# Optimization experiments

Hardware: AMD Instinct MI355X
Metric: run time of the kernel (lower is better)

Reference implementation:

```python
import jax, jax.numpy as jnp
import numpy as np

B, S, E = 4, 2048, 512
H, D = 8, 64
MIN_W, MAX_W = 256, 1024
EPS = 1e-6


def setup_inputs() -> dict:
    key = jax.random.key(0)
    ks = jax.random.split(key, 9)
    w = lambda k, shp: jax.random.normal(k, shp, dtype=jnp.float32) * 0.02
    return {
        "x": jax.random.normal(ks[0], (B, S, E), dtype=jnp.float32),
        "rms1_w": jnp.ones((E,), jnp.float32),
        "rms2_w": jnp.ones((E,), jnp.float32),
        "qkv_w": w(ks[1], (3 * E, E)),
        "out_w": w(ks[2], (E, E)),
        "cs_w1": w(ks[3], (E // 4, E)),
        "cs_w2": w(ks[4], (1, E // 4)),
        "gate_w": w(ks[5], (2304, E)),
        "up_w": w(ks[6], (2304, E)),
        "down_w": w(ks[7], (E, 2304)),
    }


def _rmsnorm(x, w):
    rms = jax.lax.rsqrt(jnp.mean(x * x, axis=-1, keepdims=True) + EPS)
    return x * rms * w


def _rotate_half(x):
    x1 = x[..., ::2]
    x2 = x[..., 1::2]
    return jnp.stack((-x2, x1), axis=-1).reshape(x.shape)


def reference(x, rms1_w, rms2_w, qkv_w, out_w, cs_w1, cs_w2, gate_w, up_w, down_w):
    # --- pre-norm ---
    h = _rmsnorm(x, rms1_w)                                  # [B,S,E]
    # --- qkv ---
    qkv = h @ qkv_w.T                                        # [B,S,3E]
    qkv = qkv.reshape(B, S, 3, H, D).transpose(2, 0, 3, 1, 4)
    q, k, v = qkv[0], qkv[1], qkv[2]                         # [B,H,S,D]
    # --- RoPE (cat-freqs cos/sin + interleaved rotate_half, as in source) ---
    inv_freq = 1.0 / (10000.0 ** (jnp.arange(0, D, 2, dtype=jnp.float32) / D))
    pos = jnp.arange(S, dtype=jnp.float32)
    freqs = jnp.outer(pos, inv_freq)                         # [S,D/2]
    emb = jnp.concatenate([freqs, freqs], axis=-1)           # [S,D]
    cos = jnp.cos(emb)[None, None]
    sin = jnp.sin(emb)[None, None]
    q = q * cos + _rotate_half(q) * sin
    k = k * cos + _rotate_half(k) * sin
    # --- attention scores ---
    scale = D ** -0.5
    scores = jnp.einsum("bhqd,bhkd->bhqk", q, k) * scale     # [B,H,S,S]
    # --- complexity -> dynamic window size ---
    n = S * E
    mu = jnp.mean(h, axis=(1, 2), keepdims=True)
    var = jnp.sum((h - mu) ** 2, axis=(1, 2)) / (n - 1)      # unbiased, per batch
    var_norm = jax.nn.sigmoid(var * 10.0 - 5.0)
    xm = jnp.mean(h, axis=1)                                 # [B,E]
    learned = jax.nn.sigmoid((jax.nn.silu(xm @ cs_w1.T)) @ cs_w2.T)[:, 0]
    complexity = (var_norm + learned) / 2.0                  # [B]
    ws_f = MIN_W + jnp.mean(complexity) * (MAX_W - MIN_W)
    ws = ws_f.astype(jnp.int32)                              # trunc, like .int()
    ws = jnp.maximum(jnp.minimum(ws, S), MIN_W)
    # --- causal + sliding-window mask ---
    p = jnp.arange(S)
    rel = p[:, None] - p[None, :]                            # [S,S]
    allowed = (rel >= 0) & (rel < ws)
    scores = jnp.where(allowed[None, None], scores, -jnp.inf)
    attn = jax.nn.softmax(scores, axis=-1)
    out = jnp.einsum("bhqk,bhkd->bhqd", attn, v)             # [B,H,S,D]
    out = out.transpose(0, 2, 1, 3).reshape(B, S, E)
    out = out @ out_w.T
    x = x + out
    # --- SwiGLU FFN ---
    h2 = _rmsnorm(x, rms2_w)
    ffn = (jax.nn.silu(h2 @ gate_w.T) * (h2 @ up_w.T)) @ down_w.T
    return x + ffn
```

## Files before the change

### kernel.cpp

```cpp
#include <hip/hip_runtime.h>

typedef unsigned short u16;
typedef unsigned int   u32;
typedef __attribute__((ext_vector_type(4))) float  f32x4;
typedef __attribute__((ext_vector_type(8))) __bf16 bf16x8;
typedef __attribute__((ext_vector_type(4))) u32    u32x4;
typedef __attribute__((ext_vector_type(2))) u32    u32x2;

#define B_ 4
#define S_ 2048
#define E_ 512
#define H_ 8
#define D_ 64

__device__ __forceinline__ u16 f2bf(float f) {
  union { float f; u32 u; } a; a.f = f;
  u32 r = a.u + 0x7FFFu + ((a.u >> 16) & 1u);
  return (u16)(r >> 16);
}
__device__ __forceinline__ float bf2f(u16 u) {
  union { u32 u; float f; } a; a.u = (u32)u << 16;
  return a.f;
}
__device__ __forceinline__ u32 pkbf(float lo, float hi) {
  u32 r;
  asm("v_cvt_pk_bf16_f32 %0, %1, %2" : "=v"(r) : "v"(lo), "v"(hi));
  return r;
}

#define GLOAD16(gp, lp) __builtin_amdgcn_global_load_lds( \
    (const __attribute__((address_space(1))) void*)(gp),  \
    (__attribute__((address_space(3))) void*)(lp), 16, 0, 0)

#define BARRIER() asm volatile("s_barrier" ::: "memory")

__global__ __launch_bounds__(256) void cvt_k(const float* __restrict__ s,
                                             u16* __restrict__ d, int n) {
  int i = (blockIdx.x * 256 + threadIdx.x) * 4;
  if (i >= n) return;
  f32x4 v = *(const f32x4*)(s + i);
  u32x2 o;
  o.x = pkbf(v[0], v[1]);
  o.y = pkbf(v[2], v[3]);
  *(u32x2*)(d + i) = o;
}

__global__ __launch_bounds__(256) void ropetab_k(float* __restrict__ ct,
                                                 float* __restrict__ st) {
  int idx = blockIdx.x * 256 + threadIdx.x;
  int s = idx >> 6, j = idx & 63;
  float f = powf(10000.f, -(float)(j & 31) * (1.f / 32.f));
  float ang = (float)s * f;
  ct[idx] = cosf(ang);
  st[idx] = sinf(ang);
}

__global__ __launch_bounds__(256) void rmsnorm_k(const float* __restrict__ x,
                                                 const float* __restrict__ wv,
                                                 u16* __restrict__ o) {
  const int row = blockIdx.x;
  const int t = threadIdx.x;
  const float* xr = x + (size_t)row * E_;
  float v0 = xr[t], v1 = xr[t + 256];
  float ss = v0 * v0 + v1 * v1;
#pragma unroll
  for (int m = 1; m < 64; m <<= 1) ss += __shfl_xor(ss, m, 64);
  __shared__ float red[4];
  if ((t & 63) == 0) red[t >> 6] = ss;
  __syncthreads();
  float tot = red[0] + red[1] + red[2] + red[3];
  float rms = 1.f / sqrtf(tot * (1.f / (float)E_) + 1e-6f);
  o[(size_t)row * E_ + t]       = f2bf(v0 * rms * wv[t]);
  o[(size_t)row * E_ + t + 256] = f2bf(v1 * rms * wv[t + 256]);
}

__global__ __launch_bounds__(256) void colsum_k(const u16* __restrict__ h,
                                                float* __restrict__ st) {
  const int b = blockIdx.x >> 3, ck = blockIdx.x & 7;
  const u16* hb = h + ((size_t)b * S_ + ck * 256) * E_;
  const int t = threadIdx.x;
  float a0 = 0, a1 = 0, s = 0, sq = 0;
  for (int r = 0; r < 256; ++r) {
    float v0 = bf2f(hb[(size_t)r * E_ + t]);
    float v1 = bf2f(hb[(size_t)r * E_ + t + 256]);
    a0 += v0; a1 += v1;
    s += v0 + v1; sq += v0 * v0 + v1 * v1;
  }
  atomicAdd(&st[8 + b * E_ + t], a0);
  atomicAdd(&st[8 + b * E_ + t + 256], a1);
#pragma unroll
  for (int m = 1; m < 64; m <<= 1) { s += __shfl_xor(s, m, 64); sq += __shfl_xor(sq, m, 64); }
  if ((t & 63) == 0) { atomicAdd(&st[b], s); atomicAdd(&st[4 + b], sq); }
}

__global__ __launch_bounds__(128) void wscalc_k(float* __restrict__ st,
                                                const float* __restrict__ w1,
                                                const float* __restrict__ w2) {
  const int j = threadIdx.x;
  __shared__ float comp[4];
  __shared__ float tw[2];
  float dot[4] = {0.f, 0.f, 0.f, 0.f};
  const float* w1r = w1 + (size_t)j * E_;
  for (int e = 0; e < E_; ++e) {
    float wv = w1r[e];
    dot[0] += st[8 + 0 * E_ + e] * wv;
    dot[1] += st[8 + 1 * E_ + e] * wv;
    dot[2] += st[8 + 2 * E_ + e] * wv;
    dot[3] += st[8 + 3 * E_ + e] * wv;
  }
  for (int b = 0; b < 4; ++b) {
    float d = dot[b] * (1.f / (float)S_);
    float si = d / (1.f + __expf(-d));
    float term = si * w2[j];
#pragma unroll
    for (int m = 1; m < 64; m <<= 1) term += __shfl_xor(term, m, 64);
    __syncthreads();
    if ((j & 63) == 0) tw[j >> 6] = term;
    __syncthreads();
    if (j == 0) {
      float pre = tw[0] + tw[1];
      float learned = 1.f / (1.f + __expf(-pre));
      const float n = (float)S_ * (float)E_;
      float sum = st[b], ssq = st[4 + b];
      float var = (ssq - sum * sum / n) / (n - 1.f);
      float vn = 1.f / (1.f + __expf(-(var * 10.f - 5.f)));
      comp[b] = 0.5f * (vn + learned);
    }
    __syncthreads();
  }
  if (j == 0) {
    float mean = 0.25f * (comp[0] + comp[1] + comp[2] + comp[3]);
    float wsf = 256.f + mean * 768.f;
    int v = (int)wsf;
    v = v < 256 ? 256 : (v > S_ ? S_ : v);
    ((int*)st)[2056] = v;
  }
}

struct EpiArgs {
  u16* q; u16* k; u16* vt;
  const float* cosT; const float* sinT;
  const float* resid; float* outf;
};

template <int N, int K, int EPI, int WAVES>
__global__ __launch_bounds__(WAVES * 64) void gemm_k(const u16* __restrict__ A,
                                                     const u16* __restrict__ W,
                                                     EpiArgs ea) {
  constexpr int NBN = N / 128;
  __shared__ u16 sA[2][128 * 32];
  __shared__ u16 sB[2][128 * 32];
  const int tid = threadIdx.x;
  const int nwg = (int)gridDim.x;
  const int bid = (int)blockIdx.x;
  const int logical = (bid & 7) * (nwg >> 3) + (bid >> 3);
  const int bm = logical / NBN, bn = logical % NBN;
  const int lane = tid & 63, w = tid >> 6;
  const int g = lane >> 4, c = lane & 15;
  constexpr int MI = (WAVES == 4) ? 4 : 2;
  const int wrow = (w >> 1) * ((WAVES == 4) ? 64 : 32);
  const int wcol = (w & 1) * 64;

  const int sr0 = w * 16 + (lane >> 2);
  const int ch0 = (lane & 3) ^ ((sr0 >> 1) & 3);
  const u16* gA = A + (size_t)(bm * 128 + sr0) * K + ch0 * 8;
  const u16* gB = W + (size_t)(bn * 128 + sr0) * K + ch0 * 8;
  const int lofs = w * 1024;

  f32x4 acc[MI][4];
  f32x4 zz = {0.f, 0.f, 0.f, 0.f};
#pragma unroll
  for (int i = 0; i < MI; ++i)
#pragma unroll
    for (int j = 0; j < 4; ++j) acc[i][j] = zz;

  auto stage = [&](int buf, int ko) {
    GLOAD16(gA + ko, (char*)sA[buf] + lofs);
    GLOAD16(gB + ko, (char*)sB[buf] + lofs);
    if constexpr (WAVES == 4) {
      GLOAD16(gA + (size_t)64 * K + ko, (char*)sA[buf] + lofs + 4096);
      GLOAD16(gB + (size_t)64 * K + ko, (char*)sB[buf] + lofs + 4096);
    }
  };

  constexpr int NIT = K / 32;
  stage(0, 0);
  int cur = 0;
  for (int it = 0; it < NIT; ++it) {
    if (it + 1 < NIT) {
      stage(cur ^ 1, (it + 1) * 32);
      if constexpr (WAVES == 4) asm volatile("s_waitcnt vmcnt(4)" ::: "memory");
      else                      asm volatile("s_waitcnt vmcnt(2)" ::: "memory");
    } else {
      asm volatile("s_waitcnt vmcnt(0)" ::: "memory");
    }
    BARRIER();
    const u16* bufA = sA[cur];
    const u16* bufB = sB[cur];
    bf16x8 af[MI], bfr[4];
#pragma unroll
    for (int mi = 0; mi < MI; ++mi) {
      int ar = wrow + mi * 16 + c;
      af[mi] = *(const bf16x8*)&bufA[ar * 32 + ((g ^ ((ar >> 1) & 3)) * 8)];
    }
#pragma unroll
    for (int nj = 0; nj < 4; ++nj) {
      int br = wcol + nj * 16 + c;
      bfr[nj] = *(const bf16x8*)&bufB[br * 32 + ((g ^ ((br >> 1) & 3)) * 8)];
    }
#pragma unroll
    for (int mi = 0; mi < MI; ++mi)
#pragma unroll
      for (int nj = 0; nj < 4; ++nj)
        acc[mi][nj] = __builtin_amdgcn_mfma_f32_16x16x32_bf16(af[mi], bfr[nj], acc[mi][nj], 0, 0, 0);
    BARRIER();
    cur ^= 1;
  }

#pragma unroll
  for (int mi = 0; mi < MI; ++mi) {
#pragma unroll
    for (int nj = 0; nj < 4; ++nj) {
      const int rowb = bm * 128 + wrow + mi * 16 + 4 * g;
      const int cc = bn * 128 + wcol + nj * 16 + c;
      if constexpr (EPI == 0) {
        const int which = cc >> 9;
        const int hh = (cc >> 6) & 7;
        const int d = cc & 63;
        const int bi = rowb >> 11;
        const int s = rowb & (S_ - 1);
        if (which == 2) {
          u32x2 pk;
          pk.x = pkbf(acc[mi][nj][0], acc[mi][nj][1]);
          pk.y = pkbf(acc[mi][nj][2], acc[mi][nj][3]);
          *(u32x2*)(ea.vt + (((size_t)(bi * H_ + hh) * D_ + d) * S_ + s)) = pk;
        } else {
          u16* dst = (which == 0 ? ea.q : ea.k) + (((size_t)(bi * H_ + hh) * S_ + s) * D_ + d);
#pragma unroll
          for (int r = 0; r < 4; ++r) {
            float v = acc[mi][nj][r];
            float pv = __shfl_xor(v, 1, 64);
            int si = s + r;
            float cs = ea.cosT[si * 64 + d];
            float sn = ea.sinT[si * 64 + d];
            float o = v * cs + ((d & 1) ? pv : -pv) * sn;
            dst[(size_t)r * D_] = f2bf(o);
          }
        }
      } else {
#pragma unroll
        for (int r = 0; r < 4; ++r) {
          size_t idx = (size_t)(rowb + r) * N + cc;
          ea.outf[idx] = acc[mi][nj][r] + ea.resid[idx];
        }
      }
    }
  }
}

__global__ __launch_bounds__(512) void gemmgu_k(const u16* __restrict__ A,
                                                const u16* __restrict__ Wg,
                                                const u16* __restrict__ Wu,
                                                u16* __restrict__ outb) {
  __shared__ u16 sA[2][128 * 32];
  __shared__ u16 sG[2][128 * 32];
  __shared__ u16 sU[2][128 * 32];
  const int tid = threadIdx.x;
  const int nwg = (int)gridDim.x;
  const int bid = (int)blockIdx.x;
  const int logical = (bid & 7) * (nwg >> 3) + (bid >> 3);
  const int bm = logical / 18, bn = logical % 18;
  const int lane = tid & 63, w = tid >> 6;
  const int g = lane >> 4, c = lane & 15;
  const int wrow = (w >> 1) * 32;
  const int wcol = (w & 1) * 64;

  const int sr0 = w * 16 + (lane >> 2);
  const int ch0 = (lane & 3) ^ ((sr0 >> 1) & 3);
  const u16* gA = A + (size_t)(bm * 128 + sr0) * 512 + ch0 * 8;
  const u16* gG = Wg + (size_t)(bn * 128 + sr0) * 512 + ch0 * 8;
  const u16* gU = Wu + (size_t)(bn * 128 + sr0) * 512 + ch0 * 8;
  const int lofs = w * 1024;

  f32x4 accg[2][4], accu[2][4];
  f32x4 zz = {0.f, 0.f, 0.f, 0.f};
#pragma unroll
  for (int i = 0; i < 2; ++i)
#pragma unroll
    for (int j = 0; j < 4; ++j) { accg[i][j] = zz; accu[i][j] = zz; }

  auto stage = [&](int buf, int ko) {
    GLOAD16(gA + ko, (char*)sA[buf] + lofs);
    GLOAD16(gG + ko, (char*)sG[buf] + lofs);
    GLOAD16(gU + ko, (char*)sU[buf] + lofs);
  };

  stage(0, 0);
  int cur = 0;
  for (int it = 0; it < 16; ++it) {
    if (it + 1 < 16) {
      stage(cur ^ 1, (it + 1) * 32);
      asm volatile("s_waitcnt vmcnt(3)" ::: "memory");
    } else {
      asm volatile("s_waitcnt vmcnt(0)" ::: "memory");
    }
    BARRIER();
    const u16* bufA = sA[cur];
    const u16* bufG = sG[cur];
    const u16* bufU = sU[cur];
    bf16x8 af[2], bg[4], bu[4];
#pragma unroll
    for (int mi = 0; mi < 2; ++mi) {
      int ar = wrow + mi * 16 + c;
      af[mi] = *(const bf16x8*)&bufA[ar * 32 + ((g ^ ((ar >> 1) & 3)) * 8)];
    }
#pragma unroll
    for (int nj = 0; nj < 4; ++nj) {
      int br = wcol + nj * 16 + c;
      int sw = (g ^ ((br >> 1) & 3)) * 8;
      bg[nj] = *(const bf16x8*)&bufG[br * 32 + sw];
      bu[nj] = *(const bf16x8*)&bufU[br * 32 + sw];
    }
#pragma unroll
    for (int mi = 0; mi < 2; ++mi)
#pragma unroll
      for (int nj = 0; nj < 4; ++nj) {
        accg[mi][nj] = __builtin_amdgcn_mfma_f32_16x16x32_bf16(af[mi], bg[nj], accg[mi][nj], 0, 0, 0);
        accu[mi][nj] = __builtin_amdgcn_mfma_f32_16x16x32_bf16(af[mi], bu[nj], accu[mi][nj], 0, 0, 0);
      }
    BARRIER();
    cur ^= 1;
  }

#pragma unroll
  for (int mi = 0; mi < 2; ++mi) {
#pragma unroll
    for (int nj = 0; nj < 4; ++nj) {
      const int rowb = bm * 128 + wrow + mi * 16 + 4 * g;
      const int cc = bn * 128 + wcol + nj * 16 + c;
#pragma unroll
      for (int r = 0; r < 4; ++r) {
        float gv = accg[mi][nj][r];
        float uv = accu[mi][nj][r];
        float sil = gv / (1.f + __expf(-gv));
        outb[(size_t)(rowb + r) * 2304 + cc] = f2bf(sil * uv);
      }
    }
  }
}

__global__ __launch_bounds__(128) void attn_k(const u16* __restrict__ Qb,
                                              const u16* __restrict__ Kb,
                                              const u16* __restrict__ Vt,
                                              u16* __restrict__ ao,
                                              const int* __restrict__ wsp) {
  const int bid = (int)blockIdx.x;
  const int qh = 63 - (bid >> 5);
  const int bh = bid & 31;
  const int b = bh >> 3, h = bh & 7;
  const int tid = threadIdx.x;
  const int w = tid >> 6, lane = tid & 63;
  const int g = lane >> 4, c = lane & 15;
  const int ws = *wsp;
  const int qw = qh * 32 + w * 16;
  const u16* Qh = Qb + (size_t)bh * S_ * D_;
  const u16* Kh = Kb + (size_t)bh * S_ * D_;
  const u16* Vh = Vt + (size_t)bh * D_ * S_;

  bf16x8 qf0 = *(const bf16x8*)(Qh + (qw + c) * D_ + g * 8);
  bf16x8 qf1 = *(const bf16x8*)(Qh + (qw + c) * D_ + 32 + g * 8);

  const float SCL = 0.125f * 1.44269504089f;
  float m2 = -3e38f, lsum = 0.f;
  f32x4 O[4];
  f32x4 zz = {0.f, 0.f, 0.f, 0.f};
#pragma unroll
  for (int i = 0; i < 4; ++i) O[i] = zz;

  int lo = qw - ws + 1;
  if (lo < 0) lo = 0;
  const int q = qw + c;
  for (int kb = lo & ~63; kb <= qw + 15; kb += 64) {
    bf16x8 kf[4][2];
#pragma unroll
    for (int t = 0; t < 4; ++t) {
      const u16* kp = Kh + (kb + 16 * t + c) * D_;
      kf[t][0] = *(const bf16x8*)(kp + g * 8);
      kf[t][1] = *(const bf16x8*)(kp + 32 + g * 8);
    }
    f32x4 st4[4];
    __builtin_amdgcn_s_setprio(1);
#pragma unroll
    for (int t = 0; t < 4; ++t) {
      f32x4 s = zz;
      s = __builtin_amdgcn_mfma_f32_16x16x32_bf16(kf[t][0], qf0, s, 0, 0, 0);
      s = __builtin_amdgcn_mfma_f32_16x16x32_bf16(kf[t][1], qf1, s, 0, 0, 0);
      st4[t] = s;
    }
    __builtin_amdgcn_s_setprio(0);
    bf16x8 vf[4][2];
#pragma unroll
    for (int dt = 0; dt < 4; ++dt) {
      const u16* vp = Vh + (size_t)(dt * 16 + c) * S_ + kb;
      vf[dt][0] = *(const bf16x8*)(vp + g * 8);
      vf[dt][1] = *(const bf16x8*)(vp + 32 + g * 8);
    }
    const bool interior = (kb + 63 <= qw) && (kb >= qw + 16 - ws);
    float p[4][4];
    float bm = -3e38f;
    if (interior) {
#pragma unroll
      for (int t = 0; t < 4; ++t)
#pragma unroll
        for (int r = 0; r < 4; ++r) {
          p[t][r] = st4[t][r] * SCL;
          bm = fmaxf(bm, p[t][r]);
        }
    } else {
#pragma unroll
      for (int t = 0; t < 4; ++t)
#pragma unroll
        for (int r = 0; r < 4; ++r) {
          int ki = kb + 16 * t + 4 * g + r;
          float v = st4[t][r] * SCL;
          bool ok = (q >= ki) && (q - ki) < ws;
          p[t][r] = ok ? v : -__builtin_inff();
          bm = fmaxf(bm, p[t][r]);
        }
    }
    bm = fmaxf(bm, __shfl_xor(bm, 16, 64));
    bm = fmaxf(bm, __shfl_xor(bm, 32, 64));
    if (!__all(bm - m2 <= 8.f)) {
      float mnew = fmaxf(m2, bm);
      float al = exp2f(m2 - mnew);
      lsum *= al;
#pragma unroll
      for (int i = 0; i < 4; ++i) O[i] *= al;
      m2 = mnew;
    }
    float psum = 0.f;
#pragma unroll
    for (int t = 0; t < 4; ++t)
#pragma unroll
      for (int r = 0; r < 4; ++r) {
        p[t][r] = exp2f(p[t][r] - m2);
        psum += p[t][r];
      }
    psum += __shfl_xor(psum, 16, 64);
    psum += __shfl_xor(psum, 32, 64);
    lsum += psum;

    u32 pp[4][2];
#pragma unroll
    for (int t = 0; t < 4; ++t) {
      pp[t][0] = pkbf(p[t][0], p[t][1]);
      pp[t][1] = pkbf(p[t][2], p[t][3]);
    }
    const int lA = (g & 1) * 32 + c;
    const int lB = lA + 16;
    const int hi = g >> 1;
    union { bf16x8 v; u32 u[4]; } pf0, pf1;
#pragma unroll
    for (int wi = 0; wi < 2; ++wi) {
      u32 a0 = (u32)__shfl((int)pp[0][wi], lA, 64);
      u32 a1 = (u32)__shfl((int)pp[1][wi], lA, 64);
      u32 a2 = (u32)__shfl((int)pp[2][wi], lA, 64);
      u32 a3 = (u32)__shfl((int)pp[3][wi], lA, 64);
      u32 b0 = (u32)__shfl((int)pp[0][wi], lB, 64);
      u32 b1 = (u32)__shfl((int)pp[1][wi], lB, 64);
      u32 b2 = (u32)__shfl((int)pp[2][wi], lB, 64);
      u32 b3 = (u32)__shfl((int)pp[3][wi], lB, 64);
      pf0.u[wi]     = hi ? a1 : a0;
      pf0.u[2 + wi] = hi ? b1 : b0;
      pf1.u[wi]     = hi ? a3 : a2;
      pf1.u[2 + wi] = hi ? b3 : b2;
    }
    __builtin_amdgcn_s_setprio(1);
#pragma unroll
    for (int dt = 0; dt < 4; ++dt) {
      O[dt] = __builtin_amdgcn_mfma_f32_16x16x32_bf16(vf[dt][0], pf0.v, O[dt], 0, 0, 0);
      O[dt] = __builtin_amdgcn_mfma_f32_16x16x32_bf16(vf[dt][1], pf1.v, O[dt], 0, 0, 0);
    }
    __builtin_amdgcn_s_setprio(0);
  }

  float inv = 1.f / lsum;
  __shared__ u16 ob[2][16][80];
#pragma unroll
  for (int dt = 0; dt < 4; ++dt)
#pragma unroll
    for (int r = 0; r < 4; ++r)
      ob[w][c][dt * 16 + 4 * g + r] = f2bf(O[dt][r] * inv);
  __syncthreads();
#pragma unroll
  for (int it = 0; it < 2; ++it) {
    int linear = tid + it * 128;
    int qrow = linear >> 3, ch = linear & 7;
    u32x4 v = *(const u32x4*)&ob[qrow >> 4][qrow & 15][ch * 8];
    *(u32x4*)(ao + ((size_t)(b * S_ + qh * 32 + qrow)) * E_ + h * D_ + ch * 8) = v;
  }
}

extern "C" void kernel_launch(void* const* d_in, const int* in_sizes, int n_in,
                              void* d_out, int out_size, void* d_ws, size_t ws_size,
                              hipStream_t stream) {
  const float* x      = (const float*)d_in[0];
  const float* rms1_w = (const float*)d_in[1];
  const float* rms2_w = (const float*)d_in[2];
  const float* qkv_w  = (const float*)d_in[3];
  const float* out_w  = (const float*)d_in[4];
  const float* cs_w1  = (const float*)d_in[5];
  const float* cs_w2  = (const float*)d_in[6];
  const float* gate_w = (const float*)d_in[7];
  const float* up_w   = (const float*)d_in[8];
  const float* down_w = (const float*)d_in[9];

  char* ws = (char*)d_ws;
  constexpr size_t o_wqkv = 0;
  constexpr size_t o_wout = 1572864;
  constexpr size_t o_wgate = 2097152;
  constexpr size_t o_wup = 4456448;
  constexpr size_t o_wdown = 6815744;
  constexpr size_t o_h = 9175040;
  constexpr size_t o_stats = 17563648;
  constexpr size_t o_cos = 17580032;
  constexpr size_t o_sin = 18104320;
  constexpr size_t o_Q = 18628608;
  constexpr size_t o_K = 27017216;
  constexpr size_t o_Vt = 35405824;
  constexpr size_t o_x2 = 43794432;
  constexpr size_t o_gate = 60571648;

  u16* wqkv = (u16*)(ws + o_wqkv);
  u16* wout = (u16*)(ws + o_wout);
  u16* wgate = (u16*)(ws + o_wgate);
  u16* wup = (u16*)(ws + o_wup);
  u16* wdown = (u16*)(ws + o_wdown);
  u16* h = (u16*)(ws + o_h);
  float* stats = (float*)(ws + o_stats);
  float* cosT = (float*)(ws + o_cos);
  float* sinT = (float*)(ws + o_sin);
  u16* Qb = (u16*)(ws + o_Q);
  u16* Kb = (u16*)(ws + o_K);
  u16* Vt = (u16*)(ws + o_Vt);
  float* x2 = (float*)(ws + o_x2);
  u16* gateb = (u16*)(ws + o_gate);
  u16* attno = h;
  u16* h2 = Qb;

  hipMemsetAsync(stats, 0, 16384, stream);
  cvt_k<<<768, 256, 0, stream>>>(qkv_w, wqkv, 1536 * 512);
  cvt_k<<<256, 256, 0, stream>>>(out_w, wout, 512 * 512);
  cvt_k<<<1152, 256, 0, stream>>>(gate_w, wgate, 2304 * 512);
  cvt_k<<<1152, 256, 0, stream>>>(up_w, wup, 2304 * 512);
  cvt_k<<<1152, 256, 0, stream>>>(down_w, wdown, 512 * 2304);
  ropetab_k<<<512, 256, 0, stream>>>(cosT, sinT);

  rmsnorm_k<<<8192, 256, 0, stream>>>(x, rms1_w, h);
  colsum_k<<<32, 256, 0, stream>>>(h, stats);
  wscalc_k<<<1, 128, 0, stream>>>(stats, cs_w1, cs_w2);

  EpiArgs ea{};
  ea.q = Qb; ea.k = Kb; ea.vt = Vt; ea.cosT = cosT; ea.sinT = sinT;
  gemm_k<1536, 512, 0, 4><<<768, 256, 0, stream>>>(h, wqkv, ea);

  attn_k<<<2048, 128, 0, stream>>>(Qb, Kb, Vt, attno, (const int*)(stats + 2056));

  EpiArgs e2{};
  e2.resid = x; e2.outf = x2;
  gemm_k<512, 512, 1, 8><<<256, 512, 0, stream>>>(attno, wout, e2);

  rmsnorm_k<<<8192, 256, 0, stream>>>(x2, rms2_w, h2);

  gemmgu_k<<<1152, 512, 0, stream>>>(h2, wgate, wup, gateb);

  EpiArgs e5{};
  e5.resid = x2; e5.outf = (float*)d_out;
  gemm_k<512, 2304, 1, 8><<<256, 512, 0, stream>>>(gateb, wdown, e5);

  (void)in_sizes; (void)n_in; (void)out_size; (void)ws_size;
}
```

Measured before the change: 397.0 us.

## Merge prep kernels, widen GEMM K-tile to 64, stage attention K/V in LDS

Merges the five weight-conversion launches and the RoPE table launch into one prep kernel. The GEMM now always runs 8 waves with a 64-wide K step, a double-buffered LDS tile and an XOR swizzle, which halves the number of barrier iterations. Attention moves to 64-query blocks of 4 waves that share K/V tiles staged through double-buffered LDS with async global-to-LDS loads, where before each wave read K/V straight from global memory. The trade-offs are more LDS per block, an extra barrier and full vmcnt wait per K block, and fewer attention blocks in the grid.

```diff
diff --git a/kernel.cpp b/kernel.cpp
--- a/kernel.cpp
+++ b/kernel.cpp
@@ -34,25 +34,37 @@
 
 #define BARRIER() asm volatile("s_barrier" ::: "memory")
 
-__global__ __launch_bounds__(256) void cvt_k(const float* __restrict__ s,
-                                             u16* __restrict__ d, int n) {
-  int i = (blockIdx.x * 256 + threadIdx.x) * 4;
-  if (i >= n) return;
+__global__ __launch_bounds__(256) void prep_k(const float* __restrict__ qkv_w,
+                                              const float* __restrict__ out_w,
+                                              const float* __restrict__ gate_w,
+                                              const float* __restrict__ up_w,
+                                              const float* __restrict__ down_w,
+                                              u16* __restrict__ wqkv, u16* __restrict__ wout,
+                                              u16* __restrict__ wgate, u16* __restrict__ wup,
+                                              u16* __restrict__ wdown,
+                                              float* __restrict__ ct, float* __restrict__ st) {
+  int bid = (int)blockIdx.x;
+  const float* s; u16* d; int base;
+  if (bid < 768)       { s = qkv_w;  d = wqkv;  base = bid; }
+  else if (bid < 1024) { s = out_w;  d = wout;  base = bid - 768; }
+  else if (bid < 2176) { s = gate_w; d = wgate; base = bid - 1024; }
+  else if (bid < 3328) { s = up_w;   d = wup;   base = bid - 2176; }
+  else if (bid < 4480) { s = down_w; d = wdown; base = bid - 3328; }
+  else {
+    int idx = (bid - 4480) * 256 + threadIdx.x;
+    int sp = idx >> 6, j = idx & 63;
+    float f = powf(10000.f, -(float)(j & 31) * (1.f / 32.f));
+    float ang = (float)sp * f;
+    ct[idx] = cosf(ang);
+    st[idx] = sinf(ang);
+    return;
+  }
+  int i = (base * 256 + threadIdx.x) * 4;
   f32x4 v = *(const f32x4*)(s + i);
   u32x2 o;
   o.x = pkbf(v[0], v[1]);
   o.y = pkbf(v[2], v[3]);
   *(u32x2*)(d + i) = o;
-}
-
-__global__ __launch_bounds__(256) void ropetab_k(float* __restrict__ ct,
-                                                 float* __restrict__ st) {
-  int idx = blockIdx.x * 256 + threadIdx.x;
-  int s = idx >> 6, j = idx & 63;
-  float f = powf(10000.f, -(float)(j & 31) * (1.f / 32.f));
-  float ang = (float)s * f;
-  ct[idx] = cosf(ang);
-  st[idx] = sinf(ang);
 }
 
 __global__ __launch_bounds__(256) void rmsnorm_k(const float* __restrict__ x,
@@ -143,13 +155,13 @@
   const float* resid; float* outf;
 };
 
-template <int N, int K, int EPI, int WAVES>
-__global__ __launch_bounds__(WAVES * 64) void gemm_k(const u16* __restrict__ A,
-                                                     const u16* __restrict__ W,
-                                                     EpiArgs ea) {
+template <int N, int K, int EPI>
+__global__ __launch_bounds__(512) void gemm_k(const u16* __restrict__ A,
+                                              const u16* __restrict__ W,
+                                              EpiArgs ea) {
   constexpr int NBN = N / 128;
-  __shared__ u16 sA[2][128 * 32];
-  __shared__ u16 sB[2][128 * 32];
+  __shared__ u16 sA[2][128 * 64];
+  __shared__ u16 sB[2][128 * 64];
   const int tid = threadIdx.x;
   const int nwg = (int)gridDim.x;
   const int bid = (int)blockIdx.x;
@@ -157,68 +169,69 @@
   const int bm = logical / NBN, bn = logical % NBN;
   const int lane = tid & 63, w = tid >> 6;
   const int g = lane >> 4, c = lane & 15;
-  constexpr int MI = (WAVES == 4) ? 4 : 2;
-  const int wrow = (w >> 1) * ((WAVES == 4) ? 64 : 32);
+  const int wrow = (w >> 1) * 32;
   const int wcol = (w & 1) * 64;
 
-  const int sr0 = w * 16 + (lane >> 2);
-  const int ch0 = (lane & 3) ^ ((sr0 >> 1) & 3);
-  const u16* gA = A + (size_t)(bm * 128 + sr0) * K + ch0 * 8;
-  const u16* gB = W + (size_t)(bn * 128 + sr0) * K + ch0 * 8;
-  const int lofs = w * 1024;
-
-  f32x4 acc[MI][4];
+  const int lr0 = lane >> 3;
+  const int scol = ((lane & 7) ^ lr0) * 8;
+  const u16* gA = A + (size_t)(bm * 128 + w * 16 + lr0) * K + scol;
+  const u16* gB = W + (size_t)(bn * 128 + w * 16 + lr0) * K + scol;
+
+  f32x4 acc[2][4];
   f32x4 zz = {0.f, 0.f, 0.f, 0.f};
 #pragma unroll
-  for (int i = 0; i < MI; ++i)
+  for (int i = 0; i < 2; ++i)
 #pragma unroll
     for (int j = 0; j < 4; ++j) acc[i][j] = zz;
 
   auto stage = [&](int buf, int ko) {
-    GLOAD16(gA + ko, (char*)sA[buf] + lofs);
-    GLOAD16(gB + ko, (char*)sB[buf] + lofs);
-    if constexpr (WAVES == 4) {
-      GLOAD16(gA + (size_t)64 * K + ko, (char*)sA[buf] + lofs + 4096);
-      GLOAD16(gB + (size_t)64 * K + ko, (char*)sB[buf] + lofs + 4096);
-    }
+    GLOAD16(gA + ko,                (char*)sA[buf] + (w * 16) * 128);
+    GLOAD16(gA + (size_t)8 * K + ko, (char*)sA[buf] + (w * 16 + 8) * 128);
+    GLOAD16(gB + ko,                (char*)sB[buf] + (w * 16) * 128);
+    GLOAD16(gB + (size_t)8 * K + ko, (char*)sB[buf] + (w * 16 + 8) * 128);
   };
 
-  constexpr int NIT = K / 32;
+  constexpr int NIT = K / 64;
   stage(0, 0);
   int cur = 0;
   for (int it = 0; it < NIT; ++it) {
     if (it + 1 < NIT) {
-      stage(cur ^ 1, (it + 1) * 32);
-      if constexpr (WAVES == 4) asm volatile("s_waitcnt vmcnt(4)" ::: "memory");
-      else                      asm volatile("s_waitcnt vmcnt(2)" ::: "memory");
+      stage(cur ^ 1, (it + 1) * 64);
+      asm volatile("s_waitcnt vmcnt(4)" ::: "memory");
     } else {
       asm volatile("s_waitcnt vmcnt(0)" ::: "memory");
     }
     BARRIER();
     const u16* bufA = sA[cur];
     const u16* bufB = sB[cur];
-    bf16x8 af[MI], bfr[4];
-#pragma unroll
-    for (int mi = 0; mi < MI; ++mi) {
+    bf16x8 af[2][2], bfr[4][2];
+#pragma unroll
+    for (int mi = 0; mi < 2; ++mi) {
       int ar = wrow + mi * 16 + c;
-      af[mi] = *(const bf16x8*)&bufA[ar * 32 + ((g ^ ((ar >> 1) & 3)) * 8)];
+#pragma unroll
+      for (int kk = 0; kk < 2; ++kk)
+        af[mi][kk] = *(const bf16x8*)&bufA[ar * 64 + (((kk * 4 + g) ^ (ar & 7)) * 8)];
     }
 #pragma unroll
     for (int nj = 0; nj < 4; ++nj) {
       int br = wcol + nj * 16 + c;
-      bfr[nj] = *(const bf16x8*)&bufB[br * 32 + ((g ^ ((br >> 1) & 3)) * 8)];
-    }
-#pragma unroll
-    for (int mi = 0; mi < MI; ++mi)
-#pragma unroll
-      for (int nj = 0; nj < 4; ++nj)
-        acc[mi][nj] = __builtin_amdgcn_mfma_f32_16x16x32_bf16(af[mi], bfr[nj], acc[mi][nj], 0, 0, 0);
+#pragma unroll
+      for (int kk = 0; kk < 2; ++kk)
+        bfr[nj][kk] = *(const bf16x8*)&bufB[br * 64 + (((kk * 4 + g) ^ (br & 7)) * 8)];
+    }
+#pragma unroll
+    for (int kk = 0; kk < 2; ++kk)
+#pragma unroll
+      for (int mi = 0; mi < 2; ++mi)
+#pragma unroll
+        for (int nj = 0; nj < 4; ++nj)
+          acc[mi][nj] = __builtin_amdgcn_mfma_f32_16x16x32_bf16(af[mi][kk], bfr[nj][kk], acc[mi][nj], 0, 0, 0);
     BARRIER();
     cur ^= 1;
   }
 
 #pragma unroll
-  for (int mi = 0; mi < MI; ++mi) {
+  for (int mi = 0; mi < 2; ++mi) {
 #pragma unroll
     for (int nj = 0; nj < 4; ++nj) {
       const int rowb = bm * 128 + wrow + mi * 16 + 4 * g;
@@ -349,26 +362,33 @@
   }
 }
 
-__global__ __launch_bounds__(128) void attn_k(const u16* __restrict__ Qb,
+__global__ __launch_bounds__(256) void attn_k(const u16* __restrict__ Qb,
                                               const u16* __restrict__ Kb,
                                               const u16* __restrict__ Vt,
                                               u16* __restrict__ ao,
                                               const int* __restrict__ wsp) {
+  __shared__ u16 sK[2][64 * 64];
+  __shared__ u16 sV[2][64 * 64];
   const int bid = (int)blockIdx.x;
-  const int qh = 63 - (bid >> 5);
+  const int qt = 31 - (bid >> 5);
   const int bh = bid & 31;
   const int b = bh >> 3, h = bh & 7;
   const int tid = threadIdx.x;
   const int w = tid >> 6, lane = tid & 63;
   const int g = lane >> 4, c = lane & 15;
   const int ws = *wsp;
-  const int qw = qh * 32 + w * 16;
+  const int qw = qt * 64 + w * 16;
   const u16* Qh = Qb + (size_t)bh * S_ * D_;
   const u16* Kh = Kb + (size_t)bh * S_ * D_;
   const u16* Vh = Vt + (size_t)bh * D_ * S_;
 
   bf16x8 qf0 = *(const bf16x8*)(Qh + (qw + c) * D_ + g * 8);
   bf16x8 qf1 = *(const bf16x8*)(Qh + (qw + c) * D_ + 32 + g * 8);
+
+  const int lr0 = lane >> 3;
+  const int scol = ((lane & 7) ^ lr0) * 8;
+  const u16* gK = Kh + (size_t)(w * 16 + lr0) * D_ + scol;
+  const u16* gV = Vh + (size_t)(w * 16 + lr0) * S_ + scol;
 
   const float SCL = 0.125f * 1.44269504089f;
   float m2 = -3e38f, lsum = 0.f;
@@ -377,127 +397,139 @@
 #pragma unroll
   for (int i = 0; i < 4; ++i) O[i] = zz;
 
-  int lo = qw - ws + 1;
-  if (lo < 0) lo = 0;
+  int lo_w = qw - ws + 1;
+  if (lo_w < 0) lo_w = 0;
+  int lo_blk = qt * 64 - ws + 1;
+  if (lo_blk < 0) lo_blk = 0;
+  lo_blk &= ~63;
+  const int qhi = qt * 64 + 63;
+  const int nkb = (qhi - lo_blk) / 64 + 1;
   const int q = qw + c;
-  for (int kb = lo & ~63; kb <= qw + 15; kb += 64) {
-    bf16x8 kf[4][2];
-#pragma unroll
-    for (int t = 0; t < 4; ++t) {
-      const u16* kp = Kh + (kb + 16 * t + c) * D_;
-      kf[t][0] = *(const bf16x8*)(kp + g * 8);
-      kf[t][1] = *(const bf16x8*)(kp + 32 + g * 8);
-    }
-    f32x4 st4[4];
-    __builtin_amdgcn_s_setprio(1);
-#pragma unroll
-    for (int t = 0; t < 4; ++t) {
-      f32x4 s = zz;
-      s = __builtin_amdgcn_mfma_f32_16x16x32_bf16(kf[t][0], qf0, s, 0, 0, 0);
-      s = __builtin_amdgcn_mfma_f32_16x16x32_bf16(kf[t][1], qf1, s, 0, 0, 0);
-      st4[t] = s;
-    }
-    __builtin_amdgcn_s_setprio(0);
-    bf16x8 vf[4][2];
-#pragma unroll
-    for (int dt = 0; dt < 4; ++dt) {
-      const u16* vp = Vh + (size_t)(dt * 16 + c) * S_ + kb;
-      vf[dt][0] = *(const bf16x8*)(vp + g * 8);
-      vf[dt][1] = *(const bf16x8*)(vp + 32 + g * 8);
-    }
-    const bool interior = (kb + 63 <= qw) && (kb >= qw + 16 - ws);
-    float p[4][4];
-    float bm = -3e38f;
-    if (interior) {
+
+  auto stageKV = [&](int buf, int kb) {
+    GLOAD16(gK + (size_t)kb * D_,            (char*)sK[buf] + (w * 16) * 128);
+    GLOAD16(gK + (size_t)(kb + 8) * D_,      (char*)sK[buf] + (w * 16 + 8) * 128);
+    GLOAD16(gV + kb,                         (char*)sV[buf] + (w * 16) * 128);
+    GLOAD16(gV + kb + (size_t)8 * S_,        (char*)sV[buf] + (w * 16 + 8) * 128);
+  };
+
+  stageKV(0, lo_blk);
+  asm volatile("s_waitcnt vmcnt(0)" ::: "memory");
+  BARRIER();
+  int cur = 0;
+  for (int i = 0; i < nkb; ++i) {
+    const int kb = lo_blk + i * 64;
+    if (i + 1 < nkb) stageKV(cur ^ 1, kb + 64);
+    if (kb <= qw + 15 && kb + 63 >= lo_w) {
+      const u16* bK = sK[cur];
+      const u16* bV = sV[cur];
+      f32x4 st4[4];
+      __builtin_amdgcn_s_setprio(1);
+#pragma unroll
+      for (int t = 0; t < 4; ++t) {
+        const int kr = 16 * t + c;
+        bf16x8 k0 = *(const bf16x8*)&bK[kr * 64 + ((g ^ (kr & 7)) * 8)];
+        bf16x8 k1 = *(const bf16x8*)&bK[kr * 64 + (((4 + g) ^ (kr & 7)) * 8)];
+        f32x4 s = zz;
+        s = __builtin_amdgcn_mfma_f32_16x16x32_bf16(k0, qf0, s, 0, 0, 0);
+        s = __builtin_amdgcn_mfma_f32_16x16x32_bf16(k1, qf1, s, 0, 0, 0);
+        st4[t] = s;
+      }
+      __builtin_amdgcn_s_setprio(0);
+      const bool interior = (kb + 63 <= qw) && (kb >= qw + 16 - ws);
+      float p[4][4];
+      float bm = -3e38f;
+      if (interior) {
+#pragma unroll
+        for (int t = 0; t < 4; ++t)
+#pragma unroll
+          for (int r = 0; r < 4; ++r) {
+            p[t][r] = st4[t][r] * SCL;
+            bm = fmaxf(bm, p[t][r]);
+          }
+      } else {
+#pragma unroll
+        for (int t = 0; t < 4; ++t)
+#pragma unroll
+          for (int r = 0; r < 4; ++r) {
+            int ki = kb + 16 * t + 4 * g + r;
+            float v = st4[t][r] * SCL;
+            bool ok = (q >= ki) && (q - ki) < ws;
+            p[t][r] = ok ? v : -__builtin_inff();
+            bm = fmaxf(bm, p[t][r]);
+          }
+      }
+      bm = fmaxf(bm, __shfl_xor(bm, 16, 64));
+      bm = fmaxf(bm, __shfl_xor(bm, 32, 64));
+      if (!__all(bm - m2 <= 8.f)) {
+        float mnew = fmaxf(m2, bm);
+        float al = exp2f(m2 - mnew);
+        lsum *= al;
+#pragma unroll
+        for (int ii = 0; ii < 4; ++ii) O[ii] *= al;
+        m2 = mnew;
+      }
+      float psum = 0.f;
 #pragma unroll
       for (int t = 0; t < 4; ++t)
 #pragma unroll
         for (int r = 0; r < 4; ++r) {
-          p[t][r] = st4[t][r] * SCL;
-          bm = fmaxf(bm, p[t][r]);
+          p[t][r] = exp2f(p[t][r] - m2);
+          psum += p[t][r];
         }
-    } else {
-#pragma unroll
-      for (int t = 0; t < 4; ++t)
-#pragma unroll
-        for (int r = 0; r < 4; ++r) {
-          int ki = kb + 16 * t + 4 * g + r;
-          float v = st4[t][r] * SCL;
-          bool ok = (q >= ki) && (q - ki) < ws;
-          p[t][r] = ok ? v : -__builtin_inff();
-          bm = fmaxf(bm, p[t][r]);
-        }
-    }
-    bm = fmaxf(bm, __shfl_xor(bm, 16, 64));
-    bm = fmaxf(bm, __shfl_xor(bm, 32, 64));
-    if (!__all(bm - m2 <= 8.f)) {
-      float mnew = fmaxf(m2, bm);
-      float al = exp2f(m2 - mnew);
-      lsum *= al;
-#pragma unroll
-      for (int i = 0; i < 4; ++i) O[i] *= al;
-      m2 = mnew;
-    }
-    float psum = 0.f;
-#pragma unroll
-    for (int t = 0; t < 4; ++t)
-#pragma unroll
-      for (int r = 0; r < 4; ++r) {
-        p[t][r] = exp2f(p[t][r] - m2);
-        psum += p[t][r];
-      }
-    psum += __shfl_xor(psum, 16, 64);
-    psum += __shfl_xor(psum, 32, 64);
-    lsum += psum;
-
-    u32 pp[4][2];
-#pragma unroll
-    for (int t = 0; t < 4; ++t) {
-      pp[t][0] = pkbf(p[t][0], p[t][1]);
-      pp[t][1] = pkbf(p[t][2], p[t][3]);
-    }
-    const int lA = (g & 1) * 32 + c;
-    const int lB = lA + 16;
-    const int hi = g >> 1;
-    union { bf16x8 v; u32 u[4]; } pf0, pf1;
-#pragma unroll
-    for (int wi = 0; wi < 2; ++wi) {
-      u32 a0 = (u32)__shfl((int)pp[0][wi], lA, 64);
-      u32 a1 = (u32)__shfl((int)pp[1][wi], lA, 64);
-      u32 a2 = (u32)__shfl((int)pp[2][wi], lA, 64);
-      u32 a3 = (u32)__shfl((int)pp[3][wi], lA, 64);
-      u32 b0 = (u32)__shfl((int)pp[0][wi], lB, 64);
-      u32 b1 = (u32)__shfl((int)pp[1][wi], lB, 64);
-      u32 b2 = (u32)__shfl((int)pp[2][wi], lB, 64);
-      u32 b3 = (u32)__shfl((int)pp[3][wi], lB, 64);
-      pf0.u[wi]     = hi ? a1 : a0;
-      pf0.u[2 + wi] = hi ? b1 : b0;
-      pf1.u[wi]     = hi ? a3 : a2;
-      pf1.u[2 + wi] = hi ? b3 : b2;
-    }
-    __builtin_amdgcn_s_setprio(1);
-#pragma unroll
-    for (int dt = 0; dt < 4; ++dt) {
-      O[dt] = __builtin_amdgcn_mfma_f32_16x16x32_bf16(vf[dt][0], pf0.v, O[dt], 0, 0, 0);
-      O[dt] = __builtin_amdgcn_mfma_f32_16x16x32_bf16(vf[dt][1], pf1.v, O[dt], 0, 0, 0);
-    }
-    __builtin_amdgcn_s_setprio(0);
-  }
-
-  float inv = 1.f / lsum;
-  __shared__ u16 ob[2][16][80];
-#pragma unroll
-  for (int dt = 0; dt < 4; ++dt)
-#pragma unroll
-    for (int r = 0; r < 4; ++r)
-      ob[w][c][dt * 16 + 4 * g + r] = f2bf(O[dt][r] * inv);
-  __syncthreads();
-#pragma unroll
-  for (int it = 0; it < 2; ++it) {
-    int linear = tid + it * 128;
-    int qrow = linear >> 3, ch = linear & 7;
-    u32x4 v = *(const u32x4*)&ob[qrow >> 4][qrow & 15][ch * 8];
-    *(u32x4*)(ao + ((size_t)(b * S_ + qh * 32 + qrow)) * E_ + h * D_ + ch * 8) = v;
+      psum += __shfl_xor(psum, 16, 64);
+      psum += __shfl_xor(psum, 32, 64);
+      lsum += psum;
+
+      u32 pp[4][2];
+#pragma unroll
+      for (int t = 0; t < 4; ++t) {
+        pp[t][0] = pkbf(p[t][0], p[t][1]);
+        pp[t][1] = pkbf(p[t][2], p[t][3]);
+      }
+      const int lA = (g & 1) * 32 + c;
+      const int lB = lA + 16;
+      const int hi = g >> 1;
+      union { bf16x8 v; u32 u[4]; } pf0, pf1;
+#pragma unroll
+      for (int wi = 0; wi < 2; ++wi) {
+        u32 a0 = (u32)__shfl((int)pp[0][wi], lA, 64);
+        u32 a1 = (u32)__shfl((int)pp[1][wi], lA, 64);
+        u32 a2 = (u32)__shfl((int)pp[2][wi], lA, 64);
+        u32 a3 = (u32)__shfl((int)pp[3][wi], lA, 64);
+        u32 b0 = (u32)__shfl((int)pp[0][wi], lB, 64);
+        u32 b1 = (u32)__shfl((int)pp[1][wi], lB, 64);
+        u32 b2 = (u32)__shfl((int)pp[2][wi], lB, 64);
+        u32 b3 = (u32)__shfl((int)pp[3][wi], lB, 64);
+        pf0.u[wi]     = hi ? a1 : a0;
+        pf0.u[2 + wi] = hi ? b1 : b0;
+        pf1.u[wi]     = hi ? a3 : a2;
+        pf1.u[2 + wi] = hi ? b3 : b2;
+      }
+      __builtin_amdgcn_s_setprio(1);
+#pragma unroll
+      for (int dt = 0; dt < 4; ++dt) {
+        const int vr = dt * 16 + c;
+        bf16x8 v0 = *(const bf16x8*)&bV[vr * 64 + ((g ^ (vr & 7)) * 8)];
+        bf16x8 v1 = *(const bf16x8*)&bV[vr * 64 + (((4 + g) ^ (vr & 7)) * 8)];
+        O[dt] = __builtin_amdgcn_mfma_f32_16x16x32_bf16(v0, pf0.v, O[dt], 0, 0, 0);
+        O[dt] = __builtin_amdgcn_mfma_f32_16x16x32_bf16(v1, pf1.v, O[dt], 0, 0, 0);
+      }
+      __builtin_amdgcn_s_setprio(0);
+    }
+    asm volatile("s_waitcnt vmcnt(0)" ::: "memory");
+    BARRIER();
+    cur ^= 1;
+  }
+
+  const float inv = 1.f / lsum;
+  u16* orow = ao + ((size_t)(b * S_ + qw + c)) * E_ + h * D_;
+#pragma unroll
+  for (int dt = 0; dt < 4; ++dt) {
+    u32x2 pk;
+    pk.x = pkbf(O[dt][0] * inv, O[dt][1] * inv);
+    pk.y = pkbf(O[dt][2] * inv, O[dt][3] * inv);
+    *(u32x2*)(orow + dt * 16 + 4 * g) = pk;
   }
 }
 
@@ -549,12 +581,8 @@
   u16* h2 = Qb;
 
   hipMemsetAsync(stats, 0, 16384, stream);
-  cvt_k<<<768, 256, 0, stream>>>(qkv_w, wqkv, 1536 * 512);
-  cvt_k<<<256, 256, 0, stream>>>(out_w, wout, 512 * 512);
-  cvt_k<<<1152, 256, 0, stream>>>(gate_w, wgate, 2304 * 512);
-  cvt_k<<<1152, 256, 0, stream>>>(up_w, wup, 2304 * 512);
-  cvt_k<<<1152, 256, 0, stream>>>(down_w, wdown, 512 * 2304);
-  ropetab_k<<<512, 256, 0, stream>>>(cosT, sinT);
+  prep_k<<<4992, 256, 0, stream>>>(qkv_w, out_w, gate_w, up_w, down_w,
+                                   wqkv, wout, wgate, wup, wdown, cosT, sinT);
 
   rmsnorm_k<<<8192, 256, 0, stream>>>(x, rms1_w, h);
   colsum_k<<<32, 256, 0, stream>>>(h, stats);
@@ -562,13 +590,13 @@
 
   EpiArgs ea{};
   ea.q = Qb; ea.k = Kb; ea.vt = Vt; ea.cosT = cosT; ea.sinT = sinT;
-  gemm_k<1536, 512, 0, 4><<<768, 256, 0, stream>>>(h, wqkv, ea);
-
-  attn_k<<<2048, 128, 0, stream>>>(Qb, Kb, Vt, attno, (const int*)(stats + 2056));
+  gemm_k<1536, 512, 0><<<768, 512, 0, stream>>>(h, wqkv, ea);
+
+  attn_k<<<1024, 256, 0, stream>>>(Qb, Kb, Vt, attno, (const int*)(stats + 2056));
 
   EpiArgs e2{};
   e2.resid = x; e2.outf = x2;
-  gemm_k<512, 512, 1, 8><<<256, 512, 0, stream>>>(attno, wout, e2);
+  gemm_k<512, 512, 1><<<256, 512, 0, stream>>>(attno, wout, e2);
 
   rmsnorm_k<<<8192, 256, 0, stream>>>(x2, rms2_w, h2);
 
@@ -576,7 +604,7 @@
 
   EpiArgs e5{};
   e5.resid = x2; e5.outf = (float*)d_out;
-  gemm_k<512, 2304, 1, 8><<<256, 512, 0, stream>>>(gateb, wdown, e5);
+  gemm_k<512, 2304, 1><<<256, 512, 0, stream>>>(gateb, wdown, e5);
 
   (void)in_sizes; (void)n_in; (void)out_size; (void)ws_size;
 }
```

Result: faster. 326.5 us (-17.7%).
